# Optimization experiments

Measured on AMD Instinct MI355X. Metric: run time of the kernel, lower is better.

Reference implementation:

```python
import jax, jax.numpy as jnp
import numpy as np
from jax import lax


def _conv(x, w, b):
    # x: [B,C,H,W] NCHW, w: [O,I,3,3] OIHW, SAME padding, stride 1
    y = lax.conv_general_dilated(x, w, (1, 1), 'SAME',
                                 dimension_numbers=('NCHW', 'OIHW', 'NCHW'))
    return y + b[None, :, None, None]


def _maxpool2(x):
    return lax.reduce_window(x, -jnp.inf, lax.max,
                             (1, 1, 2, 2), (1, 1, 2, 2), 'VALID')


def _squash(x):
    # x: [..., D]
    norm = jnp.sum(x * x, axis=-1, keepdims=True)
    scale = norm / (1.0 + norm) / jnp.sqrt(norm + 1e-9)
    return scale * x


def _routing(x, W):
    # x: [B, R, C]  (R routes, C in_channels); W: [N, R, C, O]
    # u_hat[b,n,r,o] = sum_c x[b,r,c] * W[n,r,c,o]
    u_hat = jnp.einsum('brc,nrco->bnro', x, W)
    B, N, R, O = u_hat.shape
    b_ij = jnp.zeros((B, N, R), dtype=u_hat.dtype)
    v = None
    for it in range(3):  # fixed 3 routing iterations
        c_ij = jax.nn.softmax(b_ij, axis=2)
        s_j = jnp.einsum('bnr,bnro->bno', c_ij, u_hat)
        v = _squash(s_j)
        if it < 2:
            b_ij = b_ij + jnp.einsum('bnro,bno->bnr', u_hat, v)
    return v  # [B, N, O]


def setup_inputs() -> dict:
    key = jax.random.key(0)
    ks = jax.random.split(key, 10)
    B = 512
    num_classes = 15
    x = jax.random.normal(ks[0], (B, 3, 64, 64), dtype=jnp.float32)

    def kaiming(k, shape, fan_in):
        return jax.random.normal(k, shape, dtype=jnp.float32) * np.sqrt(2.0 / fan_in)

    w1 = kaiming(ks[1], (8, 3, 3, 3), 3 * 9)
    b1 = jnp.zeros((8,), jnp.float32)
    w2 = kaiming(ks[2], (16, 8, 3, 3), 8 * 9)
    b2 = jnp.zeros((16,), jnp.float32)
    w3 = kaiming(ks[3], (32, 16, 3, 3), 16 * 9)
    b3 = jnp.zeros((32,), jnp.float32)
    # route_weights are torch.randn in the original (std 1.0)
    rw1 = jax.random.normal(ks[4], (32, 64, 32, 8), dtype=jnp.float32)   # primary
    rw2 = jax.random.normal(ks[5], (num_classes, 32, 8, 16), dtype=jnp.float32)  # secondary
    fc_w = kaiming(ks[6], (num_classes, 16 * num_classes), 16 * num_classes)
    fc_b = jnp.zeros((num_classes,), jnp.float32)
    return {'x': x, 'w1': w1, 'b1': b1, 'w2': w2, 'b2': b2,
            'w3': w3, 'b3': b3, 'rw1': rw1, 'rw2': rw2,
            'fc_w': fc_w, 'fc_b': fc_b}


def reference(x, w1, b1, w2, b2, w3, b3, rw1, rw2, fc_w, fc_b):
    h = _maxpool2(jax.nn.relu(_conv(x, w1, b1)))   # [B,8,32,32]
    h = _maxpool2(jax.nn.relu(_conv(h, w2, b2)))   # [B,16,16,16]
    h = _maxpool2(jax.nn.relu(_conv(h, w3, b3)))   # [B,32,8,8]
    B = h.shape[0]
    # routes = 64 spatial positions, channels = 32 capsule input features
    feats = h.reshape(B, 32, 64).transpose(0, 2, 1)  # [B, 64, 32]
    v1 = _routing(feats, rw1)   # [B, 32, 8]
    v2 = _routing(v1, rw2)      # [B, 15, 16]
    flat = v2.reshape(B, -1)    # [B, 240]
    return flat @ fc_w.T + fc_b  # [B, 15]
```

## Files before the change

### kernel.cpp

```cpp
#include <hip/hip_runtime.h>
#include <hip/hip_bf16.h>


template<int CIN, int COUT, int HIN, int NO>
__global__ __launch_bounds__(256)
void conv_relu_pool(const float* __restrict__ in, const float* __restrict__ w,
                    const float* __restrict__ bias, float* __restrict__ out)
{
    constexpr int HOUT = HIN / 2;
    constexpr int PR = HIN + 2;
    constexpr int PC = (HIN + 2 + 3) & ~3;
    constexpr int NS = HIN / 8;
    constexpr int NOP = COUT / NO;
    constexpr int NTASK = NOP * HOUT * NS;
    constexpr int XWORDS = CIN * PR * PC;
    constexpr int WWORDS = CIN * 9 * COUT;

    __shared__ float xin[CIN][PR][PC];
    __shared__ float wt[WWORDS];
    __shared__ float bl[COUT];

    const int tid = threadIdx.x;
    const int b   = blockIdx.x;

    for (int i = tid; i < XWORDS; i += 256) ((float*)xin)[i] = 0.f;
    for (int i = tid; i < WWORDS; i += 256) {
        int o = i % COUT, k = (i / COUT) % 9, c = i / (COUT * 9);
        wt[i] = w[(o * CIN + c) * 9 + k];
    }
    if (tid < COUT) bl[tid] = bias[tid];
    __syncthreads();

    const float4* gin = (const float4*)(in + (size_t)b * CIN * HIN * HIN);
    constexpr int CHUNKS = CIN * HIN * (HIN / 4);
    for (int i = tid; i < CHUNKS; i += 256) {
        float4 v = gin[i];
        int ch = i % (HIN / 4);
        int y  = (i / (HIN / 4)) % HIN;
        int c  = i / ((HIN / 4) * HIN);
        float* dst = &xin[c][y + 1][ch * 4 + 1];
        dst[0] = v.x; dst[1] = v.y; dst[2] = v.z; dst[3] = v.w;
    }
    __syncthreads();

    for (int task = tid; task < NTASK; task += 256) {
        const int s  = task % NS;
        const int py = (task / NS) % HOUT;
        const int o0 = (task / (NS * HOUT)) * NO;
        const int X0 = s * 8;

        float acc[NO][2][8];
#pragma unroll
        for (int n = 0; n < NO; ++n)
#pragma unroll
            for (int q = 0; q < 2; ++q)
#pragma unroll
                for (int j = 0; j < 8; ++j) acc[n][q][j] = 0.f;

        for (int c = 0; c < CIN; ++c) {
            float rows[4][12];
#pragma unroll
            for (int rr = 0; rr < 4; ++rr) {
                const float4* src = (const float4*)&xin[c][2 * py + rr][X0];
#pragma unroll
                for (int j = 0; j < 3; ++j) {
                    float4 v = src[j];
                    rows[rr][j * 4 + 0] = v.x; rows[rr][j * 4 + 1] = v.y;
                    rows[rr][j * 4 + 2] = v.z; rows[rr][j * 4 + 3] = v.w;
                }
            }
            const float* wc = wt + c * 9 * COUT;
#pragma unroll
            for (int ky = 0; ky < 3; ++ky) {
#pragma unroll
                for (int n = 0; n < NO; ++n) {
                    const float w0 = wc[(ky * 3 + 0) * COUT + o0 + n];
                    const float w1 = wc[(ky * 3 + 1) * COUT + o0 + n];
                    const float w2 = wc[(ky * 3 + 2) * COUT + o0 + n];
#pragma unroll
                    for (int j = 0; j < 8; ++j) {
                        acc[n][0][j] = fmaf(rows[ky][j],     w0, acc[n][0][j]);
                        acc[n][0][j] = fmaf(rows[ky][j + 1], w1, acc[n][0][j]);
                        acc[n][0][j] = fmaf(rows[ky][j + 2], w2, acc[n][0][j]);
                        acc[n][1][j] = fmaf(rows[ky + 1][j],     w0, acc[n][1][j]);
                        acc[n][1][j] = fmaf(rows[ky + 1][j + 1], w1, acc[n][1][j]);
                        acc[n][1][j] = fmaf(rows[ky + 1][j + 2], w2, acc[n][1][j]);
                    }
                }
            }
        }
#pragma unroll
        for (int n = 0; n < NO; ++n) {
            const float bv = bl[o0 + n];
            float4 ov;
            float* p = (float*)&ov;
#pragma unroll
            for (int j = 0; j < 4; ++j) {
                float m = fmaxf(fmaxf(acc[n][0][2 * j], acc[n][0][2 * j + 1]),
                                fmaxf(acc[n][1][2 * j], acc[n][1][2 * j + 1]));
                p[j] = fmaxf(m + bv, 0.f);
            }
            float* po = out + (((size_t)b * COUT + o0 + n) * HOUT + py) * HOUT + s * 4;
            *(float4*)po = ov;
        }
    }
}

__global__ __launch_bounds__(256)
void transpose_w1(const float* __restrict__ W, float* __restrict__ Wt)
{
    int idx = blockIdx.x * 256 + threadIdx.x;
    if (idx >= 32 * 32 * 64 * 2) return;
    int half = idx & 1;
    int r    = (idx >> 1) & 63;
    int c    = (idx >> 7) & 31;
    int n    = idx >> 12;
    ((float4*)Wt)[idx] =
        ((const float4*)W)[(((n * 64 + r) * 32 + c) << 1) + half];
}

__global__ __launch_bounds__(256)
void routing1_reg(const float* __restrict__ h3, const float* __restrict__ Wt,
                  float* __restrict__ v1)
{
    constexpr int C = 32, R = 64, O = 8, G = 2;
    const int lane = threadIdx.x & 63;
    const int n    = blockIdx.y * 4 + (threadIdx.x >> 6);
    const int b0   = blockIdx.x * G;

    float u[G][O];
#pragma unroll
    for (int g = 0; g < G; ++g)
#pragma unroll
        for (int o = 0; o < O; ++o) u[g][o] = 0.f;

    const float4* wp = (const float4*)Wt + (size_t)n * C * R * 2;
    const float* xb = h3 + (size_t)b0 * (C * R) + lane;

#pragma unroll 4
    for (int c = 0; c < C; ++c) {
        float xv[G];
#pragma unroll
        for (int g = 0; g < G; ++g) xv[g] = xb[(size_t)g * (C * R) + c * R];
        float4 w0 = wp[(c * R + lane) * 2];
        float4 w1 = wp[(c * R + lane) * 2 + 1];
#pragma unroll
        for (int g = 0; g < G; ++g) {
            u[g][0] = fmaf(xv[g], w0.x, u[g][0]);
            u[g][1] = fmaf(xv[g], w0.y, u[g][1]);
            u[g][2] = fmaf(xv[g], w0.z, u[g][2]);
            u[g][3] = fmaf(xv[g], w0.w, u[g][3]);
            u[g][4] = fmaf(xv[g], w1.x, u[g][4]);
            u[g][5] = fmaf(xv[g], w1.y, u[g][5]);
            u[g][6] = fmaf(xv[g], w1.z, u[g][6]);
            u[g][7] = fmaf(xv[g], w1.w, u[g][7]);
        }
    }

    float bij[G];
#pragma unroll
    for (int g = 0; g < G; ++g) bij[g] = 0.f;
    float s[G][O];

#pragma unroll
    for (int it = 0; it < 3; ++it) {
        float cc[G];
        if (it == 0) {
#pragma unroll
            for (int g = 0; g < G; ++g) cc[g] = 1.0f / 64.0f;
        } else {
#pragma unroll
            for (int g = 0; g < G; ++g) {
                float mx = bij[g];
#pragma unroll
                for (int w = 1; w < 64; w <<= 1) mx = fmaxf(mx, __shfl_xor(mx, w, 64));
                float e = __expf(bij[g] - mx);
                float sum = e;
#pragma unroll
                for (int w = 1; w < 64; w <<= 1) sum += __shfl_xor(sum, w, 64);
                cc[g] = e / sum;
            }
        }
#pragma unroll
        for (int g = 0; g < G; ++g)
#pragma unroll
            for (int o = 0; o < O; ++o) s[g][o] = cc[g] * u[g][o];
#pragma unroll
        for (int w = 1; w < 64; w <<= 1)
#pragma unroll
            for (int g = 0; g < G; ++g)
#pragma unroll
                for (int o = 0; o < O; ++o) s[g][o] += __shfl_xor(s[g][o], w, 64);
#pragma unroll
        for (int g = 0; g < G; ++g) {
            float nr = 0.f;
#pragma unroll
            for (int o = 0; o < O; ++o) nr = fmaf(s[g][o], s[g][o], nr);
            float scale = nr / (1.f + nr) / sqrtf(nr + 1e-9f);
#pragma unroll
            for (int o = 0; o < O; ++o) s[g][o] *= scale;
            if (it < 2) {
                float d = 0.f;
#pragma unroll
                for (int o = 0; o < O; ++o) d = fmaf(u[g][o], s[g][o], d);
                bij[g] += d;
            }
        }
    }
    float outv = 0.f;
#pragma unroll
    for (int g = 0; g < G; ++g)
#pragma unroll
        for (int o = 0; o < O; ++o)
            outv = (lane == g * O + o) ? s[g][o] : outv;
    if (lane < G * O)
        v1[(size_t)(b0 + (lane >> 3)) * 256 + n * 8 + (lane & 7)] = outv;
}

__global__ __launch_bounds__(256)
void routing2_fc(const float* __restrict__ v1, const float* __restrict__ W,
                 const float* __restrict__ fcw, const float* __restrict__ fcb,
                 float* __restrict__ out)
{
    constexpr int R = 32, C = 8, O = 16;
    __shared__ float vv[240];

    const int t  = threadIdx.x;
    const int b  = blockIdx.x;
    const int wv = t >> 6;
    const int lane = t & 63;
    const int nh = lane >> 5;
    const int r  = lane & 31;

    const float4* xr = (const float4*)(v1 + (size_t)b * 256 + r * 8);
    float4 x0 = xr[0], x1 = xr[1];
    float xv[8] = {x0.x, x0.y, x0.z, x0.w, x1.x, x1.y, x1.z, x1.w};

    float u[2][O];
    int nn[2];
#pragma unroll
    for (int p = 0; p < 2; ++p) {
        int n = wv * 4 + p * 2 + nh;
        nn[p] = n;
        int ncl = n < 15 ? n : 14;
        const float4* wp = (const float4*)(W + ((size_t)(ncl * R + r) * C) * O);
#pragma unroll
        for (int o = 0; o < O; ++o) u[p][o] = 0.f;
#pragma unroll
        for (int c = 0; c < C; ++c) {
#pragma unroll
            for (int j = 0; j < 4; ++j) {
                float4 w4 = wp[c * 4 + j];
                u[p][j * 4 + 0] = fmaf(xv[c], w4.x, u[p][j * 4 + 0]);
                u[p][j * 4 + 1] = fmaf(xv[c], w4.y, u[p][j * 4 + 1]);
                u[p][j * 4 + 2] = fmaf(xv[c], w4.z, u[p][j * 4 + 2]);
                u[p][j * 4 + 3] = fmaf(xv[c], w4.w, u[p][j * 4 + 3]);
            }
        }
    }

    float bij[2] = {0.f, 0.f};
    float s[2][O];
#pragma unroll
    for (int it = 0; it < 3; ++it) {
#pragma unroll
        for (int p = 0; p < 2; ++p) {
            float cc;
            if (it == 0) {
                cc = 1.0f / 32.0f;
            } else {
                float mx = bij[p];
#pragma unroll
                for (int w = 1; w < 32; w <<= 1) mx = fmaxf(mx, __shfl_xor(mx, w, 32));
                float e = __expf(bij[p] - mx);
                float sum = e;
#pragma unroll
                for (int w = 1; w < 32; w <<= 1) sum += __shfl_xor(sum, w, 32);
                cc = e / sum;
            }
#pragma unroll
            for (int o = 0; o < O; ++o) s[p][o] = cc * u[p][o];
        }
#pragma unroll
        for (int w = 1; w < 32; w <<= 1)
#pragma unroll
            for (int p = 0; p < 2; ++p)
#pragma unroll
                for (int o = 0; o < O; ++o) s[p][o] += __shfl_xor(s[p][o], w, 32);
#pragma unroll
        for (int p = 0; p < 2; ++p) {
            float nr = 0.f;
#pragma unroll
            for (int o = 0; o < O; ++o) nr = fmaf(s[p][o], s[p][o], nr);
            float scale = nr / (1.f + nr) / sqrtf(nr + 1e-9f);
#pragma unroll
            for (int o = 0; o < O; ++o) s[p][o] *= scale;
            if (it < 2) {
                float d = 0.f;
#pragma unroll
                for (int o = 0; o < O; ++o) d = fmaf(u[p][o], s[p][o], d);
                bij[p] += d;
            }
        }
    }
#pragma unroll
    for (int p = 0; p < 2; ++p) {
        float outv = 0.f;
#pragma unroll
        for (int o = 0; o < O; ++o) outv = (r == o) ? s[p][o] : outv;
        if (r < O && nn[p] < 15) vv[nn[p] * O + r] = outv;
    }
    __syncthreads();
    if (t < 240) {
        int j = t >> 4, k0 = t & 15;
        float acc = 0.f;
        for (int k = k0; k < 240; k += 16) acc = fmaf(vv[k], fcw[j * 240 + k], acc);
#pragma unroll
        for (int w = 1; w < 16; w <<= 1) acc += __shfl_xor(acc, w, 16);
        if (k0 == 0) out[(size_t)b * 15 + j] = acc + fcb[j];
    }
}

extern "C" void kernel_launch(void* const* d_in, const int* in_sizes, int n_in,
                              void* d_out, int out_size, void* d_ws, size_t ws_size,
                              hipStream_t stream) {
    const float* x    = (const float*)d_in[0];
    const float* w1   = (const float*)d_in[1];
    const float* b1   = (const float*)d_in[2];
    const float* w2   = (const float*)d_in[3];
    const float* b2   = (const float*)d_in[4];
    const float* w3   = (const float*)d_in[5];
    const float* b3   = (const float*)d_in[6];
    const float* rw1  = (const float*)d_in[7];
    const float* rw2  = (const float*)d_in[8];
    const float* fcw  = (const float*)d_in[9];
    const float* fcb  = (const float*)d_in[10];
    float* out = (float*)d_out;

    const int B = 512;
    float* ws = (float*)d_ws;
    float* h1 = ws;
    float* h2 = h1 + (size_t)B * 8 * 32 * 32;
    float* h3 = h2 + (size_t)B * 16 * 16 * 16;
    float* v1 = h3 + (size_t)B * 32 * 8 * 8;
    float* Wt = h2;

    conv_relu_pool<3, 8, 64, 4><<<B, 256, 0, stream>>>(x, w1, b1, h1);
    conv_relu_pool<8, 16, 32, 4><<<B, 256, 0, stream>>>(h1, w2, b2, h2);
    conv_relu_pool<16, 32, 16, 2><<<B, 256, 0, stream>>>(h2, w3, b3, h3);
    transpose_w1<<<(32 * 32 * 64 * 2 + 255) / 256, 256, 0, stream>>>(rw1, Wt);
    {
        dim3 grid(B / 2, 8);
        routing1_reg<<<grid, 256, 0, stream>>>(h3, Wt, v1);
    }
    routing2_fc<<<B, 256, 0, stream>>>(v1, rw2, fcw, fcb, out);
}
```

Measured before the change: 223.7 us.

## Split routing1 into batched einsum kernel and separate dynamic routing kernel

The fused routing1 kernel is split in two. The einsum kernel now processes 8 batch items per block instead of 2, so each transposed weight load is reused across more samples, and it writes u_hat to global memory. A new iteration kernel then runs the three routing iterations with 8 routes per thread, which replaces the 64-lane shuffle reductions with in-register sums plus 3-step shuffles. The cost is a 32 MB u_hat round trip through global memory and one extra launch, and the workspace layout is rearranged to make room for it.

```diff
diff --git a/kernel.cpp b/kernel.cpp
--- a/kernel.cpp
+++ b/kernel.cpp
@@ -120,10 +120,10 @@
 }
 
 __global__ __launch_bounds__(256)
-void routing1_reg(const float* __restrict__ h3, const float* __restrict__ Wt,
-                  float* __restrict__ v1)
-{
-    constexpr int C = 32, R = 64, O = 8, G = 2;
+void routing1_einsum(const float* __restrict__ h3, const float* __restrict__ Wt,
+                     float* __restrict__ uhat)
+{
+    constexpr int C = 32, R = 64, O = 8, G = 8;
     const int lane = threadIdx.x & 63;
     const int n    = blockIdx.y * 4 + (threadIdx.x >> 6);
     const int b0   = blockIdx.x * G;
@@ -156,65 +156,93 @@
             u[g][7] = fmaf(xv[g], w1.w, u[g][7]);
         }
     }
-
-    float bij[G];
-#pragma unroll
-    for (int g = 0; g < G; ++g) bij[g] = 0.f;
-    float s[G][O];
+#pragma unroll
+    for (int g = 0; g < G; ++g) {
+        float4* dst = (float4*)(uhat + (((size_t)(b0 + g) * 32 + n) * R + lane) * O);
+        dst[0] = make_float4(u[g][0], u[g][1], u[g][2], u[g][3]);
+        dst[1] = make_float4(u[g][4], u[g][5], u[g][6], u[g][7]);
+    }
+}
+
+__global__ __launch_bounds__(256)
+void routing1_iter(const float* __restrict__ uhat, float* __restrict__ v1)
+{
+    constexpr int O = 8;
+    const int t  = threadIdx.x;
+    const int b  = blockIdx.x;
+    const int n  = t >> 3;
+    const int rp = t & 7;
+
+    float u[8][O];
+    {
+        const float4* up = (const float4*)(uhat + (((size_t)b * 32 + n) * 64 + rp * 8) * O);
+#pragma unroll
+        for (int i = 0; i < 16; ++i) {
+            float4 w = up[i];
+            u[i >> 1][(i & 1) * 4 + 0] = w.x;
+            u[i >> 1][(i & 1) * 4 + 1] = w.y;
+            u[i >> 1][(i & 1) * 4 + 2] = w.z;
+            u[i >> 1][(i & 1) * 4 + 3] = w.w;
+        }
+    }
+
+    float bij[8];
+#pragma unroll
+    for (int k = 0; k < 8; ++k) bij[k] = 0.f;
+    float s[O];
 
 #pragma unroll
     for (int it = 0; it < 3; ++it) {
-        float cc[G];
+        float e[8];
+        float inv;
         if (it == 0) {
 #pragma unroll
-            for (int g = 0; g < G; ++g) cc[g] = 1.0f / 64.0f;
+            for (int k = 0; k < 8; ++k) e[k] = 1.f;
+            inv = 1.0f / 64.0f;
         } else {
-#pragma unroll
-            for (int g = 0; g < G; ++g) {
-                float mx = bij[g];
-#pragma unroll
-                for (int w = 1; w < 64; w <<= 1) mx = fmaxf(mx, __shfl_xor(mx, w, 64));
-                float e = __expf(bij[g] - mx);
-                float sum = e;
-#pragma unroll
-                for (int w = 1; w < 64; w <<= 1) sum += __shfl_xor(sum, w, 64);
-                cc[g] = e / sum;
-            }
-        }
-#pragma unroll
-        for (int g = 0; g < G; ++g)
-#pragma unroll
-            for (int o = 0; o < O; ++o) s[g][o] = cc[g] * u[g][o];
-#pragma unroll
-        for (int w = 1; w < 64; w <<= 1)
-#pragma unroll
-            for (int g = 0; g < G; ++g)
-#pragma unroll
-                for (int o = 0; o < O; ++o) s[g][o] += __shfl_xor(s[g][o], w, 64);
-#pragma unroll
-        for (int g = 0; g < G; ++g) {
-            float nr = 0.f;
-#pragma unroll
-            for (int o = 0; o < O; ++o) nr = fmaf(s[g][o], s[g][o], nr);
-            float scale = nr / (1.f + nr) / sqrtf(nr + 1e-9f);
-#pragma unroll
-            for (int o = 0; o < O; ++o) s[g][o] *= scale;
-            if (it < 2) {
+            float mx = bij[0];
+#pragma unroll
+            for (int k = 1; k < 8; ++k) mx = fmaxf(mx, bij[k]);
+#pragma unroll
+            for (int m = 1; m < 8; m <<= 1) mx = fmaxf(mx, __shfl_xor(mx, m, 64));
+            float sum = 0.f;
+#pragma unroll
+            for (int k = 0; k < 8; ++k) { e[k] = __expf(bij[k] - mx); sum += e[k]; }
+#pragma unroll
+            for (int m = 1; m < 8; m <<= 1) sum += __shfl_xor(sum, m, 64);
+            inv = 1.f / sum;
+        }
+        float ta[O];
+#pragma unroll
+        for (int o = 0; o < O; ++o) ta[o] = 0.f;
+#pragma unroll
+        for (int k = 0; k < 8; ++k)
+#pragma unroll
+            for (int o = 0; o < O; ++o) ta[o] = fmaf(e[k], u[k][o], ta[o]);
+#pragma unroll
+        for (int m = 1; m < 8; m <<= 1)
+#pragma unroll
+            for (int o = 0; o < O; ++o) ta[o] += __shfl_xor(ta[o], m, 64);
+        float nr = 0.f;
+#pragma unroll
+        for (int o = 0; o < O; ++o) { s[o] = ta[o] * inv; nr = fmaf(s[o], s[o], nr); }
+        float scale = nr / (1.f + nr) / sqrtf(nr + 1e-9f);
+#pragma unroll
+        for (int o = 0; o < O; ++o) s[o] *= scale;
+        if (it < 2) {
+#pragma unroll
+            for (int k = 0; k < 8; ++k) {
                 float d = 0.f;
 #pragma unroll
-                for (int o = 0; o < O; ++o) d = fmaf(u[g][o], s[g][o], d);
-                bij[g] += d;
-            }
-        }
-    }
-    float outv = 0.f;
-#pragma unroll
-    for (int g = 0; g < G; ++g)
-#pragma unroll
-        for (int o = 0; o < O; ++o)
-            outv = (lane == g * O + o) ? s[g][o] : outv;
-    if (lane < G * O)
-        v1[(size_t)(b0 + (lane >> 3)) * 256 + n * 8 + (lane & 7)] = outv;
+                for (int o = 0; o < O; ++o) d = fmaf(u[k][o], s[o], d);
+                bij[k] += d;
+            }
+        }
+    }
+    float outv = s[0];
+#pragma unroll
+    for (int o = 1; o < O; ++o) outv = (rp == o) ? s[o] : outv;
+    v1[(size_t)b * 256 + n * 8 + rp] = outv;
 }
 
 __global__ __launch_bounds__(256)
@@ -339,19 +367,21 @@
 
     const int B = 512;
     float* ws = (float*)d_ws;
-    float* h1 = ws;
-    float* h2 = h1 + (size_t)B * 8 * 32 * 32;
-    float* h3 = h2 + (size_t)B * 16 * 16 * 16;
-    float* v1 = h3 + (size_t)B * 32 * 8 * 8;
-    float* Wt = h2;
+    float* uhat = ws;
+    float* h1   = ws;
+    float* h2   = h1 + (size_t)B * 8 * 32 * 32;
+    float* h3   = uhat + (size_t)8388608;
+    float* v1   = h3 + (size_t)B * 32 * 8 * 8;
+    float* Wt   = v1 + (size_t)B * 256;
 
     conv_relu_pool<3, 8, 64, 4><<<B, 256, 0, stream>>>(x, w1, b1, h1);
     conv_relu_pool<8, 16, 32, 4><<<B, 256, 0, stream>>>(h1, w2, b2, h2);
     conv_relu_pool<16, 32, 16, 2><<<B, 256, 0, stream>>>(h2, w3, b3, h3);
     transpose_w1<<<(32 * 32 * 64 * 2 + 255) / 256, 256, 0, stream>>>(rw1, Wt);
     {
-        dim3 grid(B / 2, 8);
-        routing1_reg<<<grid, 256, 0, stream>>>(h3, Wt, v1);
-    }
+        dim3 grid(B / 8, 8);
+        routing1_einsum<<<grid, 256, 0, stream>>>(h3, Wt, uhat);
+    }
+    routing1_iter<<<B, 256, 0, stream>>>(uhat, v1);
     routing2_fc<<<B, 256, 0, stream>>>(v1, rw2, fcw, fcb, out);
 }
```

After: 213.4 us. 1.05x faster.
